# Performance work log

Measured on AMD Instinct MI355X. Metric: run time of the kernel, lower is better.

## Reference

```python
import jax, jax.numpy as jnp
import numpy as np
from jax.scipy.special import logsumexp

EPS_OT = 0.05      # self.eps in AttentionOT
MAX_ITER = 100     # Sinkhorn max_iter (torch early-stops; at convergence results match)


def _l2norm(x):
    # F.normalize(x, dim=-1, p=2) with eps=1e-12
    return x / jnp.maximum(jnp.linalg.norm(x, axis=-1, keepdims=True), 1e-12)


def _sinkhorn(Cmat, mu, nu, eps):
    # Cmat: (BK, M, N), mu: (BK, M), nu: (BK, N)
    log_mu = jnp.log(mu + 1e-8)
    log_nu = jnp.log(nu + 1e-8)

    def kern(u, v):
        # log Boltzmann kernel: (-C + u_i + v_j) / eps, shape (BK, M, N)
        return (-Cmat + u[..., :, None] + v[..., None, :]) / eps

    def step(carry, _):
        u, v = carry
        u = eps * (log_mu - logsumexp(kern(u, v), axis=2)) + u
        v = eps * (log_nu - logsumexp(kern(u, v), axis=1)) + v
        return (u, v), None

    u0 = jnp.zeros_like(mu)
    v0 = jnp.zeros_like(nu)
    (u, v), _ = jax.lax.scan(jax.checkpoint(step), (u0, v0), None, length=MAX_ITER)
    return jnp.exp(kern(u, v))  # transport plan T, (BK, M, N)


def setup_inputs() -> dict:
    key = jax.random.key(0)
    Nq, M, B, K, C = 64, 16, 8, 256, 512
    ks = jax.random.split(key, 8)
    s = 1.0 / np.sqrt(C)  # torch nn.Linear default init bound
    return {
        "xq": jax.random.normal(ks[0], (Nq, M, B, C), jnp.float32),
        "xk": jax.random.normal(ks[1], (B, K, C), jnp.float32),
        "xv": jax.random.normal(ks[2], (B, K, C), jnp.float32),
        "Wq": jax.random.uniform(ks[3], (C, C), jnp.float32, -s, s),
        "Wk": jax.random.uniform(ks[4], (C, C), jnp.float32, -s, s),
        "Wv": jax.random.uniform(ks[5], (C, C), jnp.float32, -s, s),
        "Wp": jax.random.uniform(ks[6], (C, C), jnp.float32, -s, s),
        "bp": jax.random.uniform(ks[7], (C,), jnp.float32, -s, s),
    }


def reference(xq, xk, xv, Wq, Wk, Wv, Wp, bp):
    Nq, M, B, C = xq.shape
    K = xk.shape[1]
    # projections (qkv_bias=False; proj has bias). dropout probs are 0 -> identity.
    q = _l2norm(xq @ Wq.T)          # (Nq, M, B, C)
    kk = _l2norm(xk @ Wk.T)         # (B, K, C)
    v = xv @ Wv.T                   # (B, K, C)
    # torch: einsum('bkc,nmbc->bnkm') then permute(0,2,3,1) -> (B,K,M,Nq)
    sim = jnp.einsum('bkc,nmbc->bkmn', kk, q).reshape(B * K, M, Nq)
    wdist = 1.0 - sim
    mu = jnp.full((B * K, M), 1.0 / M, dtype=sim.dtype)
    nu = jnp.full((B * K, Nq), 1.0 / Nq, dtype=sim.dtype)
    T = _sinkhorn(wdist, mu, nu, EPS_OT)            # (B*K, M, Nq)
    score_map = (M * Nq * sim * T).reshape(B, K, M, Nq)
    attn = T.reshape(B, K, M, Nq).transpose(3, 0, 1, 2)  # (Nq, B, K, M)
    x = jnp.einsum('nbkm,bkc->nmbc', attn, v)            # (Nq, M, B, C)
    x = x @ Wp.T + bp
    return x, score_map
```

## Files before the change

kernel.cpp:

```cpp
#include <hip/hip_runtime.h>


typedef short   short8  __attribute__((ext_vector_type(8)));
typedef float   floatx4 __attribute__((ext_vector_type(4)));
typedef unsigned int uint2e __attribute__((ext_vector_type(2)));

static __device__ __forceinline__ float fastrcp(float x) {
    return __builtin_amdgcn_rcpf(x);
}
static __device__ __forceinline__ unsigned short f2bf(float f) {
    union { float f; unsigned u; } c; c.f = f;
    unsigned r = c.u + 0x7FFF + ((c.u >> 16) & 1);
    return (unsigned short)(r >> 16);
}
static __device__ __forceinline__ float bf2f(unsigned short h) {
    union { unsigned u; float f; } c; c.u = (unsigned)h << 16;
    return c.f;
}

static __device__ __forceinline__ void gll16(const unsigned short* g, short* l) {
    __builtin_amdgcn_global_load_lds(
        (const __attribute__((address_space(1))) void*)g,
        (__attribute__((address_space(3))) void*)l, 16, 0, 0);
}

#if __has_builtin(__builtin_amdgcn_permlane16_swap)
static __device__ __forceinline__ float xadd16(float s) {
    uint2e r = __builtin_amdgcn_permlane16_swap(
        __float_as_uint(s), __float_as_uint(s), false, false);
    return __uint_as_float(r.x) + __uint_as_float(r.y);
}
#else
static __device__ __forceinline__ float xadd16(float s) {
    return s + __shfl_xor(s, 16, 64);
}
#endif
#if __has_builtin(__builtin_amdgcn_permlane32_swap)
static __device__ __forceinline__ float xadd32(float s) {
    uint2e r = __builtin_amdgcn_permlane32_swap(
        __float_as_uint(s), __float_as_uint(s), false, false);
    return __uint_as_float(r.x) + __uint_as_float(r.y);
}
#else
static __device__ __forceinline__ float xadd32(float s) {
    return s + __shfl_xor(s, 32, 64);
}
#endif

#define RRI(x, C) __builtin_amdgcn_update_dpp(0, (x), (C), 0xf, 0xf, true)
#define RRF(x, C) __int_as_float(RRI(__float_as_int(x), (C)))
#define GATH16(d, s) do { d[0] = (s);                                        \
    d[1]  = RRF((s), 0x121); d[2]  = RRF((s), 0x122);                        \
    d[3]  = RRF((s), 0x123); d[4]  = RRF((s), 0x124);                        \
    d[5]  = RRF((s), 0x125); d[6]  = RRF((s), 0x126);                        \
    d[7]  = RRF((s), 0x127); d[8]  = RRF((s), 0x128);                        \
    d[9]  = RRF((s), 0x129); d[10] = RRF((s), 0x12a);                        \
    d[11] = RRF((s), 0x12b); d[12] = RRF((s), 0x12c);                        \
    d[13] = RRF((s), 0x12d); d[14] = RRF((s), 0x12e);                        \
    d[15] = RRF((s), 0x12f); } while (0)

__global__ __launch_bounds__(256) void prep(
    const float* __restrict__ xq, const float* __restrict__ xk,
    const float* __restrict__ xv, const float* __restrict__ Wq,
    const float* __restrict__ Wk, const float* __restrict__ Wv,
    const float* __restrict__ Wp,
    unsigned short* __restrict__ xqh, unsigned short* __restrict__ xql,
    unsigned short* __restrict__ xkh, unsigned short* __restrict__ xkl,
    unsigned short* __restrict__ xvb,
    unsigned short* __restrict__ wqh, unsigned short* __restrict__ wql,
    unsigned short* __restrict__ wkh, unsigned short* __restrict__ wkl,
    unsigned short* __restrict__ wvb, unsigned short* __restrict__ wpb)
{
    const int b = blockIdx.x;
    const float* src; unsigned short *dh, *dl; long base;
    if (b < 4096)      { src = xq; dh = xqh; dl = xql;     base = (long)b * 256; }
    else if (b < 5120) { src = xk; dh = xkh; dl = xkl;     base = (long)(b - 4096) * 256; }
    else if (b < 6144) { src = xv; dh = xvb; dl = nullptr; base = (long)(b - 5120) * 256; }
    else if (b < 6400) { src = Wq; dh = wqh; dl = wql;     base = (long)(b - 6144) * 256; }
    else if (b < 6656) { src = Wk; dh = wkh; dl = wkl;     base = (long)(b - 6400) * 256; }
    else if (b < 6912) { src = Wv; dh = wvb; dl = nullptr; base = (long)(b - 6656) * 256; }
    else               { src = Wp; dh = wpb; dl = nullptr; base = (long)(b - 6912) * 256; }
    const long i = base + threadIdx.x;
    float4 v = ((const float4*)src)[i];
    ushort4 h;
    h.x = f2bf(v.x); h.y = f2bf(v.y); h.z = f2bf(v.z); h.w = f2bf(v.w);
    ((ushort4*)dh)[i] = h;
    if (dl) {
        ushort4 l;
        l.x = f2bf(v.x - bf2f(h.x)); l.y = f2bf(v.y - bf2f(h.y));
        l.z = f2bf(v.z - bf2f(h.z)); l.w = f2bf(v.w - bf2f(h.w));
        ((ushort4*)dl)[i] = l;
    }
}

__global__ __launch_bounds__(256, 2) void gemm_qkv2(
    const unsigned short* __restrict__ xqh, const unsigned short* __restrict__ xql,
    const unsigned short* __restrict__ xkh, const unsigned short* __restrict__ xkl,
    const unsigned short* __restrict__ xvb,
    const unsigned short* __restrict__ wqh, const unsigned short* __restrict__ wql,
    const unsigned short* __restrict__ wkh, const unsigned short* __restrict__ wkl,
    const unsigned short* __restrict__ wvb,
    unsigned short* __restrict__ qh, unsigned short* __restrict__ ql,
    unsigned short* __restrict__ kh, unsigned short* __restrict__ kl,
    unsigned short* __restrict__ vt)
{
    __shared__ __align__(16) short LB[17408];

    const int bx = blockIdx.x;
    const unsigned short *Ah, *Al, *Bh, *Bl;
    int seg, arow0;
    if (bx < 64)      { Ah = xqh; Al = xql; Bh = wqh; Bl = wql; arow0 = bx * 128;        seg = 0; }
    else if (bx < 80) { Ah = xkh; Al = xkl; Bh = wkh; Bl = wkl; arow0 = (bx - 64) * 128; seg = 1; }
    else              { Ah = xvb; Al = xvb; Bh = wvb; Bl = wvb; arow0 = (bx - 80) * 128; seg = 2; }
    const bool split = (seg != 2);

    const int tid  = threadIdx.x;
    const int lane = tid & 63, wv = tid >> 6;
    const int wr = (wv >> 1) * 64, wc = (wv & 1) * 64;
    const int j0 = blockIdx.y * 128;

    floatx4 acc[4][4];
#pragma unroll
    for (int i = 0; i < 4; i++)
#pragma unroll
        for (int j = 0; j < 4; j++) acc[i][j] = {0.f, 0.f, 0.f, 0.f};

    const int lrow = lane >> 2;
    const int lch  = (lane & 3) * 8;
    const int grow = 32 * wv;
    const long gA0 = (long)(arow0 + grow + lrow) * 512 + lch;
    const long gB0 = (long)(j0    + grow + lrow) * 512 + lch;
    short* const lA0 = LB + grow * 32;
    short* const lA1 = LB + (grow + 16) * 32;
    short* const lB0 = LB + 8192 + grow * 32;
    short* const lB1 = LB + 8192 + (grow + 16) * 32;
    short* const lAl0 = LB + 4096 + grow * 32;
    short* const lAl1 = LB + 4096 + (grow + 16) * 32;
    short* const lBl0 = LB + 12288 + grow * 32;
    short* const lBl1 = LB + 12288 + (grow + 16) * 32;

    const int fr = lane & 15, fq = (lane >> 4) * 8;

    for (int k0 = 0; k0 < 512; k0 += 32) {
        gll16(Ah + gA0 + k0, lA0);
        gll16(Ah + gA0 + k0 + 16 * 512, lA1);
        gll16(Bh + gB0 + k0, lB0);
        gll16(Bh + gB0 + k0 + 16 * 512, lB1);
        if (split) {
            gll16(Al + gA0 + k0, lAl0);
            gll16(Al + gA0 + k0 + 16 * 512, lAl1);
            gll16(Bl + gB0 + k0, lBl0);
            gll16(Bl + gB0 + k0 + 16 * 512, lBl1);
        }
        __syncthreads();
        short8 ah[4], bh[4];
#pragma unroll
        for (int i = 0; i < 4; i++)
            ah[i] = *(const short8*)&LB[(wr + i * 16 + fr) * 32 + fq];
#pragma unroll
        for (int j = 0; j < 4; j++)
            bh[j] = *(const short8*)&LB[8192 + (wc + j * 16 + fr) * 32 + fq];
        if (split) {
            short8 al[4], bl[4];
#pragma unroll
            for (int i = 0; i < 4; i++)
                al[i] = *(const short8*)&LB[4096 + (wr + i * 16 + fr) * 32 + fq];
#pragma unroll
            for (int j = 0; j < 4; j++)
                bl[j] = *(const short8*)&LB[12288 + (wc + j * 16 + fr) * 32 + fq];
#pragma unroll
            for (int i = 0; i < 4; i++)
#pragma unroll
                for (int j = 0; j < 4; j++) {
                    acc[i][j] = __builtin_amdgcn_mfma_f32_16x16x32_bf16(ah[i], bh[j], acc[i][j], 0, 0, 0);
                    acc[i][j] = __builtin_amdgcn_mfma_f32_16x16x32_bf16(ah[i], bl[j], acc[i][j], 0, 0, 0);
                    acc[i][j] = __builtin_amdgcn_mfma_f32_16x16x32_bf16(al[i], bh[j], acc[i][j], 0, 0, 0);
                }
        } else {
#pragma unroll
            for (int i = 0; i < 4; i++)
#pragma unroll
                for (int j = 0; j < 4; j++)
                    acc[i][j] = __builtin_amdgcn_mfma_f32_16x16x32_bf16(ah[i], bh[j], acc[i][j], 0, 0, 0);
        }
        __syncthreads();
    }

    const int cr = (lane >> 4) * 4, cc = lane & 15;
    if (seg == 2) {
        short (*S2)[136] = (short(*)[136])LB;
#pragma unroll
        for (int i = 0; i < 4; i++)
#pragma unroll
            for (int j = 0; j < 4; j++)
#pragma unroll
                for (int r = 0; r < 4; r++)
                    S2[wc + j * 16 + cc][wr + i * 16 + cr + r] =
                        (short)f2bf(acc[i][j][r]);
        __syncthreads();
        const int orow = tid >> 1;
        const int os   = (tid & 1) * 64;
        unsigned short* dst = vt + (long)(arow0 >> 8) * 131072
                            + (long)(j0 + orow) * 256 + (arow0 & 255) + os;
#pragma unroll
        for (int c8 = 0; c8 < 8; c8++)
            *(short8*)(dst + c8 * 8) = *(const short8*)&S2[orow][os + c8 * 8];
    } else {
#pragma unroll
        for (int i = 0; i < 4; i++)
#pragma unroll
            for (int j = 0; j < 4; j++) {
                const int gj = j0 + wc + j * 16 + cc;
#pragma unroll
                for (int r = 0; r < 4; r++) {
                    const int gi = arow0 + wr + i * 16 + cr + r;
                    const float v = acc[i][j][r];
                    const unsigned short h = f2bf(v);
                    const unsigned short lo = f2bf(v - bf2f(h));
                    if (seg == 0) {
                        const long orow = (long)((gi & 7) * 1024 + ((gi >> 3) & 15) * 64 + (gi >> 7));
                        qh[orow * 512 + gj] = h;
                        ql[orow * 512 + gj] = lo;
                    } else {
                        kh[(long)gi * 512 + gj] = h;
                        kl[(long)gi * 512 + gj] = lo;
                    }
                }
            }
    }
}

__global__ __launch_bounds__(256) void gemm_sim64(
    const short* __restrict__ Ah, const short* __restrict__ Al,
    const short* __restrict__ Bh, const short* __restrict__ Bl,
    float* __restrict__ Out, const float* __restrict__ rs)
{
    const int z = blockIdx.z;
    Ah += (long)z * 131072;  Al += (long)z * 131072;
    Bh += (long)z * 524288;  Bl += (long)z * 524288;
    Out += (long)z * 262144;
    const float* rsq = rs + (long)z * 1024;
    const float* rsk = rs + 8192 + (long)z * 256;

    __shared__ __align__(16) short Ash[64][40];
    __shared__ __align__(16) short Asl[64][40];
    __shared__ __align__(16) short Bsh[64][40];
    __shared__ __align__(16) short Bsl[64][40];

    const int tid  = threadIdx.x;
    const int lane = tid & 63, wv = tid >> 6;
    const int wr = (wv >> 1) * 32, wc = (wv & 1) * 32;
    const int i0 = blockIdx.x * 64, j0 = blockIdx.y * 64;

    floatx4 acc[2][2];
#pragma unroll
    for (int i = 0; i < 2; i++)
#pragma unroll
        for (int j = 0; j < 2; j++) acc[i][j] = {0.f, 0.f, 0.f, 0.f};

    const int sr = tid >> 2, sch = (tid & 3) * 8;
    const int fr = lane & 15, fq = (lane >> 4) * 8;

    for (int k0 = 0; k0 < 512; k0 += 32) {
        const long ao = (long)(i0 + sr) * 512 + k0 + sch;
        const long bo = (long)(j0 + sr) * 512 + k0 + sch;
        *(short8*)&Ash[sr][sch] = *(const short8*)(Ah + ao);
        *(short8*)&Asl[sr][sch] = *(const short8*)(Al + ao);
        *(short8*)&Bsh[sr][sch] = *(const short8*)(Bh + bo);
        *(short8*)&Bsl[sr][sch] = *(const short8*)(Bl + bo);
        __syncthreads();
        short8 ah[2], al[2], bh[2], bl[2];
#pragma unroll
        for (int i = 0; i < 2; i++) {
            ah[i] = *(const short8*)&Ash[wr + i * 16 + fr][fq];
            al[i] = *(const short8*)&Asl[wr + i * 16 + fr][fq];
        }
#pragma unroll
        for (int j = 0; j < 2; j++) {
            bh[j] = *(const short8*)&Bsh[wc + j * 16 + fr][fq];
            bl[j] = *(const short8*)&Bsl[wc + j * 16 + fr][fq];
        }
#pragma unroll
        for (int i = 0; i < 2; i++)
#pragma unroll
            for (int j = 0; j < 2; j++) {
                acc[i][j] = __builtin_amdgcn_mfma_f32_16x16x32_bf16(ah[i], bh[j], acc[i][j], 0, 0, 0);
                acc[i][j] = __builtin_amdgcn_mfma_f32_16x16x32_bf16(ah[i], bl[j], acc[i][j], 0, 0, 0);
                acc[i][j] = __builtin_amdgcn_mfma_f32_16x16x32_bf16(al[i], bh[j], acc[i][j], 0, 0, 0);
            }
        __syncthreads();
    }

    const int cr = (lane >> 4) * 4, cc = lane & 15;
#pragma unroll
    for (int i = 0; i < 2; i++)
#pragma unroll
        for (int j = 0; j < 2; j++) {
            const int gj = j0 + wc + j * 16 + cc;
            const float sq = rsq[gj];
#pragma unroll
            for (int r = 0; r < 4; r++) {
                const int gi = i0 + wr + i * 16 + cr + r;
                Out[(long)gi * 1024 + gj] = acc[i][j][r] * rsk[gi] * sq;
            }
        }
}

template <bool BIAS, bool OPERM, bool OUT_BF16>
__global__ __launch_bounds__(256) void gemm_bf16(
    const short* __restrict__ A, const short* __restrict__ B,
    const float* __restrict__ bias, void* __restrict__ OutV,
    int Kdim, int lda, int ldb, int ldo, long sA, long sB, long sO)
{
    __shared__ __align__(16) short As[128][40];
    __shared__ __align__(16) short Bs[128][40];

    const int tid  = threadIdx.x;
    const int lane = tid & 63, wv = tid >> 6;
    const int wr = (wv >> 1) * 64, wc = (wv & 1) * 64;
    const int i0 = blockIdx.x * 128, j0 = blockIdx.y * 128;

    floatx4 acc[4][4];
#pragma unroll
    for (int i = 0; i < 4; i++)
#pragma unroll
        for (int j = 0; j < 4; j++) acc[i][j] = {0.f, 0.f, 0.f, 0.f};

    const int sr = tid >> 2, sk = (tid & 3) * 8;
    const int fr = lane & 15, fq = (lane >> 4) * 8;
    const short* pa = A + (long)blockIdx.z * sA;
    const short* pb = B + (long)blockIdx.z * sB;

    for (int k0 = 0; k0 < Kdim; k0 += 32) {
#pragma unroll
        for (int p = 0; p < 2; p++) {
            *(short8*)&As[sr + p * 64][sk] =
                *(const short8*)(pa + (long)(i0 + sr + p * 64) * lda + k0 + sk);
            *(short8*)&Bs[sr + p * 64][sk] =
                *(const short8*)(pb + (long)(j0 + sr + p * 64) * ldb + k0 + sk);
        }
        __syncthreads();
        short8 af[4], bf[4];
#pragma unroll
        for (int i = 0; i < 4; i++) af[i] = *(const short8*)&As[wr + i * 16 + fr][fq];
#pragma unroll
        for (int j = 0; j < 4; j++) bf[j] = *(const short8*)&Bs[wc + j * 16 + fr][fq];
#pragma unroll
        for (int i = 0; i < 4; i++)
#pragma unroll
            for (int j = 0; j < 4; j++)
                acc[i][j] = __builtin_amdgcn_mfma_f32_16x16x32_bf16(af[i], bf[j], acc[i][j], 0, 0, 0);
        __syncthreads();
    }

    float* Of = nullptr; unsigned short* Ob = nullptr;
    if constexpr (OUT_BF16) Ob = (unsigned short*)OutV + (long)blockIdx.z * sO;
    else                    Of = (float*)OutV + (long)blockIdx.z * sO;
    const int cr = (lane >> 4) * 4, cc = lane & 15;
#pragma unroll
    for (int i = 0; i < 4; i++) {
#pragma unroll
        for (int j = 0; j < 4; j++) {
            const int gj = j0 + wc + j * 16 + cc;
            float bb = 0.0f;
            if constexpr (BIAS) bb = bias[gj];
#pragma unroll
            for (int r = 0; r < 4; r++) {
                const int gi = i0 + wr + i * 16 + cr + r;
                float v = acc[i][j][r] + bb;
                long idx;
                if constexpr (OPERM)
                    idx = (long)((gi & 63) * 128 + ((gi >> 6) & 15) * 8 + (gi >> 10)) * ldo + gj;
                else
                    idx = (long)gi * ldo + gj;
                if constexpr (OUT_BF16) Ob[idx] = f2bf(v);
                else                    Of[idx] = v;
            }
        }
    }
}

__global__ __launch_bounds__(256) void rownorm(
    const unsigned short* __restrict__ qh, const unsigned short* __restrict__ ql,
    const unsigned short* __restrict__ kh, const unsigned short* __restrict__ kl,
    float* __restrict__ rs)
{
    const int row  = blockIdx.x * 4 + (threadIdx.x >> 6);
    const int lane = threadIdx.x & 63;
    const unsigned short *ph, *pl;
    long r;
    if (row < 8192) { ph = qh; pl = ql; r = row; }
    else            { ph = kh; pl = kl; r = row - 8192; }
    const long o = r * 512 + lane * 8;
    ushort4 h0 = *(const ushort4*)(ph + o), h1 = *(const ushort4*)(ph + o + 4);
    ushort4 l0 = *(const ushort4*)(pl + o), l1 = *(const ushort4*)(pl + o + 4);
    float ss = 0.0f;
    const unsigned short hv[8] = {h0.x, h0.y, h0.z, h0.w, h1.x, h1.y, h1.z, h1.w};
    const unsigned short lv[8] = {l0.x, l0.y, l0.z, l0.w, l1.x, l1.y, l1.z, l1.w};
#pragma unroll
    for (int i = 0; i < 8; i++) {
        const float v = bf2f(hv[i]) + bf2f(lv[i]);
        ss = fmaf(v, v, ss);
    }
#pragma unroll
    for (int off = 32; off; off >>= 1) ss += __shfl_xor(ss, off, 64);
    if (lane == 0) rs[row] = 1.0f / fmaxf(sqrtf(ss), 1e-12f);
}

__global__ __launch_bounds__(256, 2) void sinkhorn5(
    const float* __restrict__ sim, float* __restrict__ score,
    unsigned short* __restrict__ Tt)
{
    const int lane = threadIdx.x & 63;
    const int bk   = blockIdx.x * 4 + (threadIdx.x >> 6);
    const float* S = sim + (long)bk * 1024;
    const int m = lane & 15, g = lane >> 4;

    int idx[16];
    idx[0] = m;
    idx[1]  = RRI(m, 0x121); idx[2]  = RRI(m, 0x122); idx[3]  = RRI(m, 0x123);
    idx[4]  = RRI(m, 0x124); idx[5]  = RRI(m, 0x125); idx[6]  = RRI(m, 0x126);
    idx[7]  = RRI(m, 0x127); idx[8]  = RRI(m, 0x128); idx[9]  = RRI(m, 0x129);
    idx[10] = RRI(m, 0x12a); idx[11] = RRI(m, 0x12b); idx[12] = RRI(m, 0x12c);
    idx[13] = RRI(m, 0x12d); idx[14] = RRI(m, 0x12e); idx[15] = RRI(m, 0x12f);

    float K1[16], K2R[16], sv[16];
#pragma unroll
    for (int j = 0; j < 16; j++) {
        K1[j] = __expf((S[m * 64 + g * 16 + idx[j]] - 1.0f) * 20.0f);
        const float s_ = S[idx[j] * 64 + lane];
        sv[j]  = s_;
        K2R[j] = __expf((s_ - 1.0f) * 20.0f);
    }

    const float muP = 0.0625f + 1e-8f;
    const float nuP = 0.015625f + 1e-8f;
    float b = 1.0f;
    float aB[16], bB[16];
#pragma unroll
    for (int j = 0; j < 16; j++) bB[j] = 1.0f;

#pragma unroll 1
    for (int it = 0; it < 100; it++) {
        float s0 = 0, s1 = 0, s2 = 0, s3 = 0;
#pragma unroll
        for (int j = 0; j < 4; j++) {
            s0 = fmaf(K1[j],      bB[j],      s0);
            s1 = fmaf(K1[4 + j],  bB[4 + j],  s1);
            s2 = fmaf(K1[8 + j],  bB[8 + j],  s2);
            s3 = fmaf(K1[12 + j], bB[12 + j], s3);
        }
        float s = (s0 + s1) + (s2 + s3);
        s = xadd16(s);
        s = xadd32(s);
        const float a = muP * fastrcp(s);
        GATH16(aB, a);
        float t0 = 0, t1 = 0, t2 = 0, t3 = 0;
#pragma unroll
        for (int j = 0; j < 4; j++) {
            t0 = fmaf(K2R[j],      aB[j],      t0);
            t1 = fmaf(K2R[4 + j],  aB[4 + j],  t1);
            t2 = fmaf(K2R[8 + j],  aB[8 + j],  t2);
            t3 = fmaf(K2R[12 + j], aB[12 + j], t3);
        }
        const float bp_ = b;
        b = nuP * fastrcp((t0 + t1) + (t2 + t3));
        GATH16(bB, b);
        const int conv = __builtin_fabsf(b - bp_) <= 1e-5f * __builtin_fabsf(b);
        if (__all(conv)) break;
    }

    float* Sc = score + (long)bk * 1024;
    unsigned short* Tp = Tt + (long)(bk >> 8) * 262144 + (bk & 255);
#pragma unroll
    for (int j = 0; j < 16; j++) {
        const int row = idx[j];
        const float Tv = aB[j] * K2R[j] * b;
        Sc[row * 64 + lane] = 1024.0f * sv[j] * Tv;
        Tp[(long)(row * 64 + lane) * 256] = f2bf(Tv);
    }
}

extern "C" void kernel_launch(void* const* d_in, const int* in_sizes, int n_in,
                              void* d_out, int out_size, void* d_ws, size_t ws_size,
                              hipStream_t stream)
{
    (void)in_sizes; (void)n_in; (void)out_size; (void)ws_size;
    const float* xq = (const float*)d_in[0];
    const float* xk = (const float*)d_in[1];
    const float* xv = (const float*)d_in[2];
    const float* Wq = (const float*)d_in[3];
    const float* Wk = (const float*)d_in[4];
    const float* Wv = (const float*)d_in[5];
    const float* Wp = (const float*)d_in[6];
    const float* bp = (const float*)d_in[7];

    float* out_x     = (float*)d_out;
    float* out_score = out_x + 8192L * 512;

    char* W = (char*)d_ws;
    const long MB = 1 << 20;
    unsigned short* qh   = (unsigned short*)(W + 0);
    unsigned short* ql   = (unsigned short*)(W + 8 * MB);
    unsigned short* xq_h = (unsigned short*)(W + 16 * MB);
    float*          simb = (float*)(W + 16 * MB);
    unsigned short* xq_l = (unsigned short*)(W + 24 * MB);
    unsigned short* xpre = (unsigned short*)(W + 24 * MB);
    unsigned short* xk_h = (unsigned short*)(W + 32 * MB);
    unsigned short* xk_l = (unsigned short*)(W + 34 * MB);
    unsigned short* Tt   = (unsigned short*)(W + 32 * MB);
    unsigned short* xv_b = (unsigned short*)(W + 36 * MB);
    unsigned short* kh   = (unsigned short*)(W + 38 * MB);
    unsigned short* kl   = (unsigned short*)(W + 40 * MB);
    unsigned short* vt   = (unsigned short*)(W + 42 * MB);
    unsigned short* wqh  = (unsigned short*)(W + 44 * MB);
    unsigned short* wql  = (unsigned short*)(W + 44 * MB + 1 * 524288);
    unsigned short* wkh  = (unsigned short*)(W + 44 * MB + 2 * 524288);
    unsigned short* wkl  = (unsigned short*)(W + 44 * MB + 3 * 524288);
    unsigned short* wvb  = (unsigned short*)(W + 44 * MB + 4 * 524288);
    unsigned short* wpb  = (unsigned short*)(W + 44 * MB + 5 * 524288);
    float*          rs   = (float*)(W + 47 * MB);

    const dim3 blk(256);

    prep<<<7168, blk, 0, stream>>>(xq, xk, xv, Wq, Wk, Wv, Wp,
                                   xq_h, xq_l, xk_h, xk_l, xv_b,
                                   wqh, wql, wkh, wkl, wvb, wpb);

    gemm_qkv2<<<dim3(96, 4), blk, 0, stream>>>(
        xq_h, xq_l, xk_h, xk_l, xv_b, wqh, wql, wkh, wkl, wvb,
        qh, ql, kh, kl, vt);

    rownorm<<<2560, blk, 0, stream>>>(qh, ql, kh, kl, rs);

    gemm_sim64<<<dim3(4, 16, 8), blk, 0, stream>>>(
        (const short*)kh, (const short*)kl, (const short*)qh, (const short*)ql,
        simb, rs);

    sinkhorn5<<<512, blk, 0, stream>>>(simb, out_score, Tt);

    gemm_bf16<false, false, true><<<dim3(8, 4, 8), blk, 0, stream>>>(
        (const short*)Tt, (const short*)vt, nullptr, xpre,
        256, 256, 256, 512, 262144, 131072, 524288);

    gemm_bf16<true, true, false><<<dim3(64, 4), blk, 0, stream>>>(
        (const short*)xpre, (const short*)wpb, bp, out_x,
        512, 512, 512, 512, 0, 0, 0);
}
```

Measured before the change: 193.4 us.

## Double-buffer LDS tiles in QKV projection GEMM to overlap loads with MFMA

```diff
diff --git a/kernel.cpp b/kernel.cpp
--- a/kernel.cpp
+++ b/kernel.cpp
@@ -104,7 +104,7 @@
     unsigned short* __restrict__ kh, unsigned short* __restrict__ kl,
     unsigned short* __restrict__ vt)
 {
-    __shared__ __align__(16) short LB[17408];
+    __shared__ __align__(16) short LB[32768];
 
     const int bx = blockIdx.x;
     const unsigned short *Ah, *Al, *Bh, *Bl;
@@ -130,44 +130,46 @@
     const int grow = 32 * wv;
     const long gA0 = (long)(arow0 + grow + lrow) * 512 + lch;
     const long gB0 = (long)(j0    + grow + lrow) * 512 + lch;
-    short* const lA0 = LB + grow * 32;
-    short* const lA1 = LB + (grow + 16) * 32;
-    short* const lB0 = LB + 8192 + grow * 32;
-    short* const lB1 = LB + 8192 + (grow + 16) * 32;
-    short* const lAl0 = LB + 4096 + grow * 32;
-    short* const lAl1 = LB + 4096 + (grow + 16) * 32;
-    short* const lBl0 = LB + 12288 + grow * 32;
-    short* const lBl1 = LB + 12288 + (grow + 16) * 32;
 
     const int fr = lane & 15, fq = (lane >> 4) * 8;
 
-    for (int k0 = 0; k0 < 512; k0 += 32) {
-        gll16(Ah + gA0 + k0, lA0);
-        gll16(Ah + gA0 + k0 + 16 * 512, lA1);
-        gll16(Bh + gB0 + k0, lB0);
-        gll16(Bh + gB0 + k0 + 16 * 512, lB1);
-        if (split) {
-            gll16(Al + gA0 + k0, lAl0);
-            gll16(Al + gA0 + k0 + 16 * 512, lAl1);
-            gll16(Bl + gB0 + k0, lBl0);
-            gll16(Bl + gB0 + k0 + 16 * 512, lBl1);
-        }
-        __syncthreads();
+#define QKV_STAGE(d, k0) do {                                                 \
+        short* bb = LB + (d) * 16384;                                         \
+        gll16(Ah + gA0 + (k0),            bb + grow * 32);                    \
+        gll16(Ah + gA0 + (k0) + 16 * 512, bb + (grow + 16) * 32);             \
+        gll16(Bh + gB0 + (k0),            bb + 8192 + grow * 32);             \
+        gll16(Bh + gB0 + (k0) + 16 * 512, bb + 8192 + (grow + 16) * 32);      \
+        if (split) {                                                          \
+            gll16(Al + gA0 + (k0),            bb + 4096 + grow * 32);         \
+            gll16(Al + gA0 + (k0) + 16 * 512, bb + 4096 + (grow + 16) * 32);  \
+            gll16(Bl + gB0 + (k0),            bb + 12288 + grow * 32);        \
+            gll16(Bl + gB0 + (k0) + 16 * 512, bb + 12288 + (grow + 16) * 32); \
+        }                                                                     \
+    } while (0)
+
+    QKV_STAGE(0, 0);
+    __syncthreads();
+
+#pragma unroll 2
+    for (int t = 0; t < 16; t++) {
+        const int cur = t & 1;
+        if (t < 15) QKV_STAGE(cur ^ 1, (t + 1) * 32);
+        const short* base = LB + cur * 16384;
         short8 ah[4], bh[4];
 #pragma unroll
         for (int i = 0; i < 4; i++)
-            ah[i] = *(const short8*)&LB[(wr + i * 16 + fr) * 32 + fq];
+            ah[i] = *(const short8*)&base[(wr + i * 16 + fr) * 32 + fq];
 #pragma unroll
         for (int j = 0; j < 4; j++)
-            bh[j] = *(const short8*)&LB[8192 + (wc + j * 16 + fr) * 32 + fq];
+            bh[j] = *(const short8*)&base[8192 + (wc + j * 16 + fr) * 32 + fq];
         if (split) {
             short8 al[4], bl[4];
 #pragma unroll
             for (int i = 0; i < 4; i++)
-                al[i] = *(const short8*)&LB[4096 + (wr + i * 16 + fr) * 32 + fq];
+                al[i] = *(const short8*)&base[4096 + (wr + i * 16 + fr) * 32 + fq];
 #pragma unroll
             for (int j = 0; j < 4; j++)
-                bl[j] = *(const short8*)&LB[12288 + (wc + j * 16 + fr) * 32 + fq];
+                bl[j] = *(const short8*)&base[12288 + (wc + j * 16 + fr) * 32 + fq];
 #pragma unroll
             for (int i = 0; i < 4; i++)
 #pragma unroll
@@ -185,6 +187,7 @@
         }
         __syncthreads();
     }
+#undef QKV_STAGE
 
     const int cr = (lane >> 4) * 4, cc = lane & 15;
     if (seg == 2) {
```

New measurement: 188.8 us. 2.4% less time.
